# Kernel tuning notes

Measured on AMD Instinct MI355X. Metric: run time of the kernel, lower is better.

The kernel has to match this reference:

```python
import jax, jax.numpy as jnp
import numpy as np

B, T, D, H = 4, 1024, 1024, 16
DH = D // H  # 64

def setup_inputs() -> dict:
    key = jax.random.key(0)
    ks = jax.random.split(key, 5)
    s = 1.0 / np.sqrt(D)
    return {
        "x": jax.random.normal(ks[0], (B, T, D), dtype=jnp.float32),
        "Wqkv": jax.random.uniform(ks[1], (D, 3 * D), dtype=jnp.float32, minval=-s, maxval=s),
        "bqkv": jax.random.uniform(ks[2], (3 * D,), dtype=jnp.float32, minval=-s, maxval=s),
        "Wproj": jax.random.uniform(ks[3], (D, D), dtype=jnp.float32, minval=-s, maxval=s),
        "bproj": jax.random.uniform(ks[4], (D,), dtype=jnp.float32, minval=-s, maxval=s),
        "mask": jnp.ones((B, T), dtype=jnp.int32),
    }

def reference(x, Wqkv, bqkv, Wproj, bproj, mask):
    Bx, Tx, C = x.shape
    qkv = x @ Wqkv + bqkv                      # [B,T,3D]
    q, k, v = jnp.split(qkv, 3, axis=-1)
    # [B,H,T,DH]
    q = q.reshape(Bx, Tx, H, DH).transpose(0, 2, 1, 3)
    k = k.reshape(Bx, Tx, H, DH).transpose(0, 2, 1, 3)
    v = v.reshape(Bx, Tx, H, DH).transpose(0, 2, 1, 3)
    att = jnp.einsum("bhqd,bhkd->bhqk", q, k) / np.sqrt(DH)
    causal = jnp.tril(jnp.ones((Tx, Tx), dtype=bool))          # [T,T]
    keep = causal[None, None] & (mask[:, None, None, :] != 0)  # [B,1,T,T] broadcast
    att = jnp.where(keep, att, -jnp.inf)
    att = jax.nn.softmax(att, axis=-1)
    # dropout is identity in eval / p=0
    out = jnp.einsum("bhqk,bhkd->bhqd", att, v)                # [B,H,T,DH]
    out = out.transpose(0, 2, 1, 3).reshape(Bx, Tx, C)
    return out @ Wproj + bproj
```

## Files before the change

### kernel.cpp

```cpp
#include <hip/hip_runtime.h>
#include <hip/hip_bf16.h>
#include <cstddef>
#include <cstdint>

#define Bb 4
#define Tt 1024
#define Dd 1024
#define Hh 16

typedef __bf16 bf16x8 __attribute__((ext_vector_type(8)));
typedef __bf16 bf16x4 __attribute__((ext_vector_type(4)));
typedef float  f32x4  __attribute__((ext_vector_type(4)));

__device__ __forceinline__ void gload16(const void* g, void* l) {
    __builtin_amdgcn_global_load_lds(
        (const __attribute__((address_space(1))) void*)g,
        (__attribute__((address_space(3))) void*)l, 16, 0, 0);
}

__global__ __launch_bounds__(256) void prep(const float* __restrict__ x,
                                            const float* __restrict__ Wqkv,
                                            const float* __restrict__ Wproj,
                                            __bf16* __restrict__ xb,
                                            __bf16* __restrict__ wqT,
                                            __bf16* __restrict__ wpT) {
    const int bid = blockIdx.x;
    if (bid < 4096) {
        int i = bid * 256 + threadIdx.x;
        float4 v = ((const float4*)x)[i];
        bf16x4 o = { (__bf16)v.x, (__bf16)v.y, (__bf16)v.z, (__bf16)v.w };
        ((bf16x4*)xb)[i] = o;
        return;
    }
    __shared__ float ld[64][65];
    const float* in;
    __bf16* out;
    int K, N, k0, n0;
    if (bid < 4096 + 768) {
        int j = bid - 4096;
        in = Wqkv; out = wqT; K = 1024; N = 3072;
        k0 = (j & 15) * 64; n0 = (j >> 4) * 64;
    } else {
        int j = bid - 4096 - 768;
        in = Wproj; out = wpT; K = 1024; N = 1024;
        k0 = (j & 15) * 64; n0 = (j >> 4) * 64;
    }
    #pragma unroll
    for (int i = 0; i < 16; i++) {
        int idx = i * 256 + threadIdx.x;
        int r = idx >> 6, c = idx & 63;
        ld[r][c] = in[(size_t)(k0 + r) * N + n0 + c];
    }
    __syncthreads();
    #pragma unroll
    for (int i = 0; i < 16; i++) {
        int idx = i * 256 + threadIdx.x;
        int r = idx >> 6, c = idx & 63;
        out[(size_t)(n0 + r) * K + k0 + c] = (__bf16)ld[c][r];
    }
}

__device__ __forceinline__ void stage_half(const __bf16* __restrict__ g,
                                           __bf16* l, int tid) {
    #pragma unroll
    for (int s = 0; s < 2; ++s) {
        const int c = s * 512 + tid;
        const int r = c >> 3;
        const int seg = (c & 7) ^ (r & 7);
        gload16(&g[(size_t)r * 1024 + seg * 8], &l[c * 8]);
    }
}

template <int MH>
__device__ __forceinline__ void load_af(bf16x8 (&af)[4][2], const __bf16* AsC,
                                        int wy, int l15, int quad) {
    #pragma unroll
    for (int mi = 0; mi < 4; ++mi)
        #pragma unroll
        for (int kc = 0; kc < 2; ++kc)
            af[mi][kc] = *(const bf16x8*)&AsC[(wy * 128 + MH * 64 + mi * 16 + l15) * 64 +
                                              (((kc * 4 + quad) ^ (l15 & 7)) * 8)];
}

template <int MH, int NH>
__device__ __forceinline__ void mfma_quad(f32x4 (&acc)[8][4], const bf16x8 (&af)[4][2],
                                          const bf16x8 (&bf)[4][2]) {
    #pragma unroll
    for (int mi = 0; mi < 4; ++mi)
        #pragma unroll
        for (int nj = 0; nj < 2; ++nj) {
            f32x4 c = acc[MH * 4 + mi][NH * 2 + nj];
            c = __builtin_amdgcn_mfma_f32_16x16x32_bf16(af[mi][0], bf[NH * 2 + nj][0], c, 0, 0, 0);
            c = __builtin_amdgcn_mfma_f32_16x16x32_bf16(af[mi][1], bf[NH * 2 + nj][1], c, 0, 0, 0);
            acc[MH * 4 + mi][NH * 2 + nj] = c;
        }
}

__global__ __launch_bounds__(512, 2) void gemm_qkv(const __bf16* __restrict__ A,
                                                   const __bf16* __restrict__ Bt,
                                                   const float* __restrict__ bias,
                                                   __bf16* __restrict__ Cout,
                                                   __bf16* __restrict__ vt) {
    constexpr int N = 3072;
    constexpr int NT = 16;
    __shared__ __align__(16) __bf16 smem[65536];

    const int tid  = threadIdx.x;
    const int lane = tid & 63;
    const int wave = tid >> 6;
    const int wy = wave >> 2, wx = wave & 3;
    const int l15 = lane & 15, quad = lane >> 4;
    const size_t row0 = (size_t)blockIdx.y * 256;
    const size_t col0 = (size_t)blockIdx.x * 256;

    const __bf16* const Ab  = A  + row0 * 1024;
    const __bf16* const Bb_ = Bt + col0 * 1024;

    f32x4 acc[8][4] = {};
    bf16x8 af[4][2], bf[4][2];

    stage_half(Ab, smem, tid);
    stage_half(Ab + (size_t)128 * 1024, smem + 8192, tid);
    stage_half(Bb_, smem + 32768, tid);
    stage_half(Bb_ + (size_t)128 * 1024, smem + 32768 + 8192, tid);
    stage_half(Bb_ + 64, smem + 32768 + 16384, tid);
    stage_half(Bb_ + (size_t)128 * 1024 + 64, smem + 32768 + 16384 + 8192, tid);
    stage_half(Ab + 64, smem + 16384, tid);
    asm volatile("s_waitcnt vmcnt(6)" ::: "memory");
    __builtin_amdgcn_s_barrier();

    for (int t = 0; t < NT; ++t) {
        const int cur = t & 1;
        __bf16* const AsC = smem + cur * 16384;
        __bf16* const BsC = smem + 32768 + cur * 16384;
        __bf16* const AsN = smem + (cur ^ 1) * 16384;

        load_af<0>(af, AsC, wy, l15, quad);
        #pragma unroll
        for (int nj = 0; nj < 4; ++nj)
            #pragma unroll
            for (int kc = 0; kc < 2; ++kc)
                bf[nj][kc] = *(const bf16x8*)&BsC[(wx * 64 + nj * 16 + l15) * 64 +
                                                  (((kc * 4 + quad) ^ (l15 & 7)) * 8)];
        if (t + 1 < NT) stage_half(Ab + (size_t)128 * 1024 + (t + 1) * 64, AsN + 8192, tid);
        __builtin_amdgcn_s_barrier();
        asm volatile("s_waitcnt lgkmcnt(0)" ::: "memory");
        __builtin_amdgcn_s_setprio(1);
        mfma_quad<0, 0>(acc, af, bf);
        __builtin_amdgcn_s_setprio(0);
        __builtin_amdgcn_s_barrier();

        if (t + 2 < NT) stage_half(Bb_ + (t + 2) * 64, BsC, tid);
        __builtin_amdgcn_s_barrier();
        asm volatile("s_waitcnt lgkmcnt(0)" ::: "memory");
        __builtin_amdgcn_s_setprio(1);
        mfma_quad<0, 1>(acc, af, bf);
        __builtin_amdgcn_s_setprio(0);
        __builtin_amdgcn_s_barrier();

        load_af<1>(af, AsC, wy, l15, quad);
        if (t + 2 < NT) stage_half(Bb_ + (size_t)128 * 1024 + (t + 2) * 64, BsC + 8192, tid);
        __builtin_amdgcn_s_barrier();
        asm volatile("s_waitcnt lgkmcnt(0)" ::: "memory");
        __builtin_amdgcn_s_setprio(1);
        mfma_quad<1, 0>(acc, af, bf);
        __builtin_amdgcn_s_setprio(0);
        __builtin_amdgcn_s_barrier();

        if (t + 2 < NT) stage_half(Ab + (t + 2) * 64, AsC, tid);
        if (t + 2 < NT) {
            asm volatile("s_waitcnt vmcnt(6)" ::: "memory");
        } else if (t + 1 < NT) {
            asm volatile("s_waitcnt vmcnt(0)" ::: "memory");
        }
        __builtin_amdgcn_s_barrier();
        asm volatile("s_waitcnt lgkmcnt(0)" ::: "memory");
        __builtin_amdgcn_s_setprio(1);
        mfma_quad<1, 1>(acc, af, bf);
        __builtin_amdgcn_s_setprio(0);
        __builtin_amdgcn_s_barrier();
    }

    const float scale = (col0 < 1024) ? 0.125f : 1.0f;
    const int isV = (col0 >= 2048);
    for (int sl = 0; sl < 2; ++sl) {
        if (wy == sl) {
            #pragma unroll
            for (int nj = 0; nj < 4; ++nj) {
                const int cl = wx * 64 + nj * 16 + l15;
                const float bj = bias[col0 + cl];
                #pragma unroll
                for (int mi = 0; mi < 8; ++mi) {
                    #pragma unroll
                    for (int r = 0; r < 4; ++r)
                        smem[(mi * 16 + quad * 4 + r) * 264 + cl] =
                            (__bf16)((acc[mi][nj][r] + bj) * scale);
                }
            }
        }
        __syncthreads();
        #pragma unroll
        for (int p = 0; p < 8; ++p) {
            const int idx = p * 512 + tid;
            const int row = idx >> 5, ch = idx & 31;
            bf16x8 v = *(const bf16x8*)&smem[row * 264 + ch * 8];
            *(bf16x8*)&Cout[(row0 + sl * 128 + row) * N + col0 + ch * 8] = v;
        }
        if (isV) {
            const int bidx = (int)(row0 >> 10);
            const int t0g  = (int)(row0 & 1023) + sl * 128;
            const int cl   = tid & 255;
            const int th   = tid >> 8;
            const int hd   = (int)(col0 - 2048) + cl;
            const size_t vrow = ((size_t)((bidx * Hh + (hd >> 6)) * 64 + (hd & 63))) * Tt + t0g;
            #pragma unroll
            for (int p = 0; p < 8; ++p) {
                const int tch = th * 8 + p;
                bf16x8 v;
                #pragma unroll
                for (int u = 0; u < 8; ++u) v[u] = smem[(tch * 8 + u) * 264 + cl];
                *(bf16x8*)&vt[vrow + tch * 8] = v;
            }
        }
        __syncthreads();
    }
}

__global__ __launch_bounds__(256) void gemm_bf16_n64(const __bf16* __restrict__ A,
                                                     const __bf16* __restrict__ Bt,
                                                     const float* __restrict__ bias,
                                                     float* __restrict__ Cout,
                                                     int M, int N, int K) {
    __shared__ __align__(16) __bf16 As[128 * 64];
    __shared__ __align__(16) __bf16 Bs[64 * 64];
    const int tid  = threadIdx.x;
    const int lane = tid & 63;
    const int wave = tid >> 6;
    const int wy = wave >> 1, wx = wave & 1;
    const int l15 = lane & 15, quad = lane >> 4;
    const size_t row0 = (size_t)blockIdx.y * 128;
    const size_t col0 = (size_t)blockIdx.x * 64;

    f32x4 acc[4][2] = {};

    for (int k0 = 0; k0 < K; k0 += 64) {
        #pragma unroll
        for (int i = 0; i < 4; i++) {
            int c = i * 256 + tid;
            int r = c >> 3, seg = (c & 7) ^ (r & 7);
            gload16(&A[(row0 + r) * K + k0 + seg * 8], &As[c * 8]);
        }
        #pragma unroll
        for (int i = 0; i < 2; i++) {
            int c = i * 256 + tid;
            int r = c >> 3, seg = (c & 7) ^ (r & 7);
            gload16(&Bt[(col0 + r) * K + k0 + seg * 8], &Bs[c * 8]);
        }
        __syncthreads();
        #pragma unroll
        for (int kc = 0; kc < 2; kc++) {
            bf16x8 af[4], bfr[2];
            #pragma unroll
            for (int i = 0; i < 4; i++)
                af[i] = *(const bf16x8*)&As[(wy * 64 + i * 16 + l15) * 64 +
                                            (((kc * 4 + quad) ^ (l15 & 7)) * 8)];
            #pragma unroll
            for (int j = 0; j < 2; j++)
                bfr[j] = *(const bf16x8*)&Bs[(wx * 32 + j * 16 + l15) * 64 +
                                             (((kc * 4 + quad) ^ (l15 & 7)) * 8)];
            #pragma unroll
            for (int i = 0; i < 4; i++)
                #pragma unroll
                for (int j = 0; j < 2; j++)
                    acc[i][j] = __builtin_amdgcn_mfma_f32_16x16x32_bf16(af[i], bfr[j], acc[i][j], 0, 0, 0);
        }
        __syncthreads();
    }

    #pragma unroll
    for (int j = 0; j < 2; j++) {
        const size_t col = col0 + wx * 32 + j * 16 + l15;
        const float bj = bias[col];
        #pragma unroll
        for (int i = 0; i < 4; i++) {
            const size_t row = row0 + wy * 64 + i * 16 + quad * 4;
            #pragma unroll
            for (int r = 0; r < 4; r++)
                Cout[(row + r) * N + col] = acc[i][j][r] + bj;
        }
    }
}

__global__ __launch_bounds__(256, 4) void attn_mfma(const __bf16* __restrict__ qkv,
                                                    const __bf16* __restrict__ vt,
                                                    const int* __restrict__ mask,
                                                    __bf16* __restrict__ att) {
    __shared__ __align__(16) __bf16 Ks[2][4096];
    __shared__ __align__(16) __bf16 Vs[2][4096];
    __shared__ __align__(16) __bf16 Ps[4][1024];

    const int h  = blockIdx.x & 15;
    const int b  = blockIdx.x >> 4;
    const int qt = 15 - blockIdx.y;
    const int tid = threadIdx.x, lane = tid & 63, wave = tid >> 6;
    const int l15 = lane & 15, quad = lane >> 4;

    #pragma unroll
    for (int i = 0; i < 2; i++) {
        int c = i * 256 + tid;
        int rr = c >> 3, ch = c & 7;
        gload16(&qkv[((size_t)(b * Tt + qt * 64 + rr)) * 3072 + h * 64 + ((ch ^ (rr & 7)) * 8)],
                &Ks[0][c * 8]);
    }

    uint32_t mlo = 0, mhi = 0;
    for (int p = 0; p < 16; p++) {
        unsigned long long bal = __ballot(mask[b * Tt + p * 64 + lane] != 0);
        if ((lane & 15) == p) { mlo = (uint32_t)bal; mhi = (uint32_t)(bal >> 32); }
    }

    __syncthreads();
    bf16x8 qf0 = *(const bf16x8*)&Ks[0][(wave * 16 + l15) * 64 + ((quad ^ (l15 & 7)) * 8)];
    bf16x8 qf1 = *(const bf16x8*)&Ks[0][(wave * 16 + l15) * 64 + (((4 + quad) ^ (l15 & 7)) * 8)];
    __syncthreads();

    #pragma unroll
    for (int i = 0; i < 2; i++) {
        int c = i * 256 + tid;
        int rr = c >> 3, ch = c & 7, sw = ((ch ^ (rr & 7)) * 8);
        gload16(&qkv[((size_t)(b * Tt + rr)) * 3072 + 1024 + h * 64 + sw], &Ks[0][c * 8]);
        gload16(&vt[((size_t)((b * Hh + h) * 64 + rr)) * Tt + sw], &Vs[0][c * 8]);
    }

    f32x4 Oacc[4] = {};
    float lsum = 0.0f;

    for (int kt = 0; kt <= qt; kt++) {
        __syncthreads();
        const int cur = kt & 1;
        if (kt < qt) {
            #pragma unroll
            for (int i = 0; i < 2; i++) {
                int c = i * 256 + tid;
                int rr = c >> 3, ch = c & 7, sw = ((ch ^ (rr & 7)) * 8);
                gload16(&qkv[((size_t)(b * Tt + (kt + 1) * 64 + rr)) * 3072 + 1024 + h * 64 + sw],
                        &Ks[cur ^ 1][c * 8]);
                gload16(&vt[((size_t)((b * Hh + h) * 64 + rr)) * Tt + (kt + 1) * 64 + sw],
                        &Vs[cur ^ 1][c * 8]);
            }
        }

        const uint32_t lo = (uint32_t)__builtin_amdgcn_readlane((int)mlo, kt);
        const uint32_t hi = (uint32_t)__builtin_amdgcn_readlane((int)mhi, kt);

        bf16x8 ak[4][2];
        #pragma unroll
        for (int j = 0; j < 4; j++)
            #pragma unroll
            for (int kc = 0; kc < 2; kc++)
                ak[j][kc] = *(const bf16x8*)&Ks[cur][(j * 16 + l15) * 64 +
                                                     (((kc * 4 + quad) ^ (l15 & 7)) * 8)];
        #pragma unroll
        for (int j = 0; j < 4; j++) {
            f32x4 st = {};
            st = __builtin_amdgcn_mfma_f32_16x16x32_bf16(ak[j][0], qf0, st, 0, 0, 0);
            st = __builtin_amdgcn_mfma_f32_16x16x32_bf16(ak[j][1], qf1, st, 0, 0, 0);
            const uint32_t fld = (j < 2) ? (lo >> (j * 16)) : (hi >> ((j - 2) * 16));
            bf16x4 pv;
            #pragma unroll
            for (int r = 0; r < 4; r++) {
                const int tloc = j * 16 + quad * 4 + r;
                bool keep = (fld >> (quad * 4 + r)) & 1;
                if (kt == qt) keep = keep && (tloc <= wave * 16 + l15);
                const float pe = keep ? __expf(st[r]) : 0.0f;
                lsum += pe;
                pv[r] = (__bf16)pe;
            }
            *(bf16x4*)&Ps[wave][l15 * 64 + (((j * 4 + quad) ^ ((l15 & 7) << 1)) * 4)] = pv;
        }

        bf16x8 av[4][2];
        #pragma unroll
        for (int n = 0; n < 4; n++)
            #pragma unroll
            for (int kc = 0; kc < 2; kc++)
                av[n][kc] = *(const bf16x8*)&Vs[cur][(n * 16 + l15) * 64 +
                                                     (((kc * 4 + quad) ^ (l15 & 7)) * 8)];
        bf16x8 p0 = *(const bf16x8*)&Ps[wave][l15 * 64 + (((2 * quad) ^ ((l15 & 7) << 1)) * 4)];
        bf16x8 p1 = *(const bf16x8*)&Ps[wave][l15 * 64 + (((2 * (4 + quad)) ^ ((l15 & 7) << 1)) * 4)];
        #pragma unroll
        for (int n = 0; n < 4; n++) {
            Oacc[n] = __builtin_amdgcn_mfma_f32_16x16x32_bf16(av[n][0], p0, Oacc[n], 0, 0, 0);
            Oacc[n] = __builtin_amdgcn_mfma_f32_16x16x32_bf16(av[n][1], p1, Oacc[n], 0, 0, 0);
        }
    }

    float lt = lsum;
    lt += __shfl_xor(lt, 16);
    lt += __shfl_xor(lt, 32);
    const float inv = 1.0f / lt;
    const int q = qt * 64 + wave * 16 + l15;
    #pragma unroll
    for (int n = 0; n < 4; n++) {
        bf16x4 o;
        #pragma unroll
        for (int r = 0; r < 4; r++) o[r] = (__bf16)(Oacc[n][r] * inv);
        *(bf16x4*)&att[((size_t)(b * Tt + q)) * Dd + h * 64 + n * 16 + quad * 4] = o;
    }
}

extern "C" void kernel_launch(void* const* d_in, const int* in_sizes, int n_in,
                              void* d_out, int out_size, void* d_ws, size_t ws_size,
                              hipStream_t stream) {
    const float* x     = (const float*)d_in[0];
    const float* Wqkv  = (const float*)d_in[1];
    const float* bqkv  = (const float*)d_in[2];
    const float* Wproj = (const float*)d_in[3];
    const float* bproj = (const float*)d_in[4];
    const int*   mask  = (const int*)d_in[5];
    float* out = (float*)d_out;

    __bf16* xb  = (__bf16*)d_ws;
    __bf16* wqT = xb  + (size_t)4096 * 1024;
    __bf16* wpT = wqT + (size_t)3072 * 1024;
    __bf16* qkv = wpT + (size_t)1024 * 1024;
    __bf16* vt  = qkv + (size_t)4096 * 3072;
    __bf16* att = vt  + (size_t)4 * 16 * 64 * 1024;

    prep<<<4096 + 768 + 256, 256, 0, stream>>>(x, Wqkv, Wproj, xb, wqT, wpT);

    gemm_qkv<<<dim3(12, 16), 512, 0, stream>>>(xb, wqT, bqkv, qkv, vt);

    attn_mfma<<<dim3(64, 16), 256, 0, stream>>>(qkv, vt, mask, att);

    gemm_bf16_n64<<<dim3(16, 32), 256, 0, stream>>>(att, wpT, bproj, out, 4096, 1024, 1024);
}
```

Before: 166.8 us.

## Software-pipeline LDS fragment loads in QKV GEMM with partial lgkmcnt waits

Restructures the QKV GEMM main loop so the A fragments for the next K-step are prefetched from LDS during the last MFMA quadrant, B fragments are split into two halves, and partial lgkmcnt waits replace full drains. Staging addresses are precomputed once and sched_barriers pin instruction order. Barriers per iteration drop, and the two B halves are now staged together. The aim is to overlap LDS reads with MFMA and cut synchronization stalls, at the cost of more registers and tighter correctness constraints on wait counts.

```diff
diff --git a/kernel.cpp b/kernel.cpp
--- a/kernel.cpp
+++ b/kernel.cpp
@@ -17,6 +17,14 @@
         (const __attribute__((address_space(1))) void*)g,
         (__attribute__((address_space(3))) void*)l, 16, 0, 0);
 }
+
+#define LGKM4() asm volatile("s_waitcnt lgkmcnt(4)" ::: "memory")
+#define LGKM8() asm volatile("s_waitcnt lgkmcnt(8)" ::: "memory")
+#define LGKM0() asm volatile("s_waitcnt lgkmcnt(0)" ::: "memory")
+#define VMC6()  asm volatile("s_waitcnt vmcnt(6)" ::: "memory")
+#define VMC0()  asm volatile("s_waitcnt vmcnt(0)" ::: "memory")
+#define SB()    __builtin_amdgcn_s_barrier()
+#define SCB()   __builtin_amdgcn_sched_barrier(0)
 
 __global__ __launch_bounds__(256) void prep(const float* __restrict__ x,
                                             const float* __restrict__ Wqkv,
@@ -60,39 +68,31 @@
     }
 }
 
-__device__ __forceinline__ void stage_half(const __bf16* __restrict__ g,
-                                           __bf16* l, int tid) {
-    #pragma unroll
-    for (int s = 0; s < 2; ++s) {
-        const int c = s * 512 + tid;
-        const int r = c >> 3;
-        const int seg = (c & 7) ^ (r & 7);
-        gload16(&g[(size_t)r * 1024 + seg * 8], &l[c * 8]);
-    }
-}
-
-template <int MH>
-__device__ __forceinline__ void load_af(bf16x8 (&af)[4][2], const __bf16* AsC,
-                                        int wy, int l15, int quad) {
+__device__ __forceinline__ void ld8(bf16x8 (&f)[4][2], const __bf16* p0, const __bf16* p1) {
+    #pragma unroll
+    for (int mi = 0; mi < 4; ++mi) {
+        f[mi][0] = *(const bf16x8*)(p0 + mi * 1024);
+        f[mi][1] = *(const bf16x8*)(p1 + mi * 1024);
+    }
+}
+__device__ __forceinline__ void ld4(bf16x8 (&f)[2][2], const __bf16* p0, const __bf16* p1) {
+    #pragma unroll
+    for (int j = 0; j < 2; ++j) {
+        f[j][0] = *(const bf16x8*)(p0 + j * 1024);
+        f[j][1] = *(const bf16x8*)(p1 + j * 1024);
+    }
+}
+template <int M0, int N0>
+__device__ __forceinline__ void mm8(f32x4 (&acc)[8][4], const bf16x8 (&AF)[4][2],
+                                    const bf16x8 (&BF)[2][2]) {
     #pragma unroll
     for (int mi = 0; mi < 4; ++mi)
         #pragma unroll
-        for (int kc = 0; kc < 2; ++kc)
-            af[mi][kc] = *(const bf16x8*)&AsC[(wy * 128 + MH * 64 + mi * 16 + l15) * 64 +
-                                              (((kc * 4 + quad) ^ (l15 & 7)) * 8)];
-}
-
-template <int MH, int NH>
-__device__ __forceinline__ void mfma_quad(f32x4 (&acc)[8][4], const bf16x8 (&af)[4][2],
-                                          const bf16x8 (&bf)[4][2]) {
-    #pragma unroll
-    for (int mi = 0; mi < 4; ++mi)
-        #pragma unroll
-        for (int nj = 0; nj < 2; ++nj) {
-            f32x4 c = acc[MH * 4 + mi][NH * 2 + nj];
-            c = __builtin_amdgcn_mfma_f32_16x16x32_bf16(af[mi][0], bf[NH * 2 + nj][0], c, 0, 0, 0);
-            c = __builtin_amdgcn_mfma_f32_16x16x32_bf16(af[mi][1], bf[NH * 2 + nj][1], c, 0, 0, 0);
-            acc[MH * 4 + mi][NH * 2 + nj] = c;
+        for (int j = 0; j < 2; ++j) {
+            f32x4 c = acc[M0 + mi][N0 + j];
+            c = __builtin_amdgcn_mfma_f32_16x16x32_bf16(AF[mi][0], BF[j][0], c, 0, 0, 0);
+            c = __builtin_amdgcn_mfma_f32_16x16x32_bf16(AF[mi][1], BF[j][1], c, 0, 0, 0);
+            acc[M0 + mi][N0 + j] = c;
         }
 }
 
@@ -116,18 +116,34 @@
     const __bf16* const Ab  = A  + row0 * 1024;
     const __bf16* const Bb_ = Bt + col0 * 1024;
 
+    const int c0 = tid, c1 = 512 + tid;
+    const int r0 = c0 >> 3, s0 = ((c0 & 7) ^ (r0 & 7));
+    const int r1 = c1 >> 3, s1 = ((c1 & 7) ^ (r1 & 7));
+    const int go0 = r0 * 1024 + s0 * 8, go1 = r1 * 1024 + s1 * 8;
+    const int lo0 = c0 * 8, lo1 = c1 * 8;
+#define STAGE(gb, lb) do { const __bf16* _g = (gb); __bf16* _l = (lb); \
+        gload16(_g + go0, _l + lo0); gload16(_g + go1, _l + lo1); } while (0)
+
+    const int x7 = l15 & 7;
+    const int ch0 = (quad ^ x7) * 8, ch1 = ((4 + quad) ^ x7) * 8;
+    const int aoff0 = (wy * 128 + l15) * 64 + ch0;
+    const int aoff1 = (wy * 128 + l15) * 64 + ch1;
+    const int boff0 = (wx * 64 + l15) * 64 + ch0;
+    const int boff1 = (wx * 64 + l15) * 64 + ch1;
+
     f32x4 acc[8][4] = {};
-    bf16x8 af[4][2], bf[4][2];
-
-    stage_half(Ab, smem, tid);
-    stage_half(Ab + (size_t)128 * 1024, smem + 8192, tid);
-    stage_half(Bb_, smem + 32768, tid);
-    stage_half(Bb_ + (size_t)128 * 1024, smem + 32768 + 8192, tid);
-    stage_half(Bb_ + 64, smem + 32768 + 16384, tid);
-    stage_half(Bb_ + (size_t)128 * 1024 + 64, smem + 32768 + 16384 + 8192, tid);
-    stage_half(Ab + 64, smem + 16384, tid);
-    asm volatile("s_waitcnt vmcnt(6)" ::: "memory");
-    __builtin_amdgcn_s_barrier();
+    bf16x8 af0[4][2], af1[4][2], bfA[2][2], bfB[2][2];
+
+    STAGE(Ab,                          smem);
+    STAGE(Ab  + (size_t)128 * 1024,    smem + 8192);
+    STAGE(Bb_,                         smem + 32768);
+    STAGE(Bb_ + (size_t)128 * 1024,    smem + 32768 + 8192);
+    STAGE(Bb_ + 64,                    smem + 32768 + 16384);
+    STAGE(Bb_ + (size_t)128 * 1024 + 64, smem + 32768 + 16384 + 8192);
+    STAGE(Ab  + 64,                    smem + 16384);
+    VMC6(); SB(); SCB();
+    ld8(af0, smem + aoff0, smem + aoff1);
+    SCB();
 
     for (int t = 0; t < NT; ++t) {
         const int cur = t & 1;
@@ -135,51 +151,48 @@
         __bf16* const BsC = smem + 32768 + cur * 16384;
         __bf16* const AsN = smem + (cur ^ 1) * 16384;
 
-        load_af<0>(af, AsC, wy, l15, quad);
-        #pragma unroll
-        for (int nj = 0; nj < 4; ++nj)
-            #pragma unroll
-            for (int kc = 0; kc < 2; ++kc)
-                bf[nj][kc] = *(const bf16x8*)&BsC[(wx * 64 + nj * 16 + l15) * 64 +
-                                                  (((kc * 4 + quad) ^ (l15 & 7)) * 8)];
-        if (t + 1 < NT) stage_half(Ab + (size_t)128 * 1024 + (t + 1) * 64, AsN + 8192, tid);
-        __builtin_amdgcn_s_barrier();
-        asm volatile("s_waitcnt lgkmcnt(0)" ::: "memory");
+        ld4(bfA, BsC + boff0, BsC + boff1);
+        SCB();
+        ld4(bfB, BsC + 2048 + boff0, BsC + 2048 + boff1);
+        if (t + 1 < NT) STAGE(Ab + (size_t)128 * 1024 + (t + 1) * 64, AsN + 8192);
+        LGKM4(); SCB();
         __builtin_amdgcn_s_setprio(1);
-        mfma_quad<0, 0>(acc, af, bf);
+        mm8<0, 0>(acc, af0, bfA);
         __builtin_amdgcn_s_setprio(0);
-        __builtin_amdgcn_s_barrier();
-
-        if (t + 2 < NT) stage_half(Bb_ + (t + 2) * 64, BsC, tid);
-        __builtin_amdgcn_s_barrier();
-        asm volatile("s_waitcnt lgkmcnt(0)" ::: "memory");
+        SB(); SCB();
+
+        ld8(af1, AsC + 4096 + aoff0, AsC + 4096 + aoff1);
+        LGKM8(); SCB();
         __builtin_amdgcn_s_setprio(1);
-        mfma_quad<0, 1>(acc, af, bf);
+        mm8<0, 2>(acc, af0, bfB);
         __builtin_amdgcn_s_setprio(0);
-        __builtin_amdgcn_s_barrier();
-
-        load_af<1>(af, AsC, wy, l15, quad);
-        if (t + 2 < NT) stage_half(Bb_ + (size_t)128 * 1024 + (t + 2) * 64, BsC + 8192, tid);
-        __builtin_amdgcn_s_barrier();
-        asm volatile("s_waitcnt lgkmcnt(0)" ::: "memory");
+        SB(); SCB();
+
+        if (t + 2 < NT) {
+            STAGE(Bb_ + (t + 2) * 64, BsC);
+            STAGE(Bb_ + (size_t)128 * 1024 + (t + 2) * 64, BsC + 8192);
+        }
+        LGKM0(); SCB();
         __builtin_amdgcn_s_setprio(1);
-        mfma_quad<1, 0>(acc, af, bf);
+        mm8<4, 0>(acc, af1, bfA);
         __builtin_amdgcn_s_setprio(0);
-        __builtin_amdgcn_s_barrier();
-
-        if (t + 2 < NT) stage_half(Ab + (t + 2) * 64, AsC, tid);
+        SB(); SCB();
+
         if (t + 2 < NT) {
-            asm volatile("s_waitcnt vmcnt(6)" ::: "memory");
+            STAGE(Ab + (t + 2) * 64, AsC);
+            VMC6();
         } else if (t + 1 < NT) {
-            asm volatile("s_waitcnt vmcnt(0)" ::: "memory");
-        }
-        __builtin_amdgcn_s_barrier();
-        asm volatile("s_waitcnt lgkmcnt(0)" ::: "memory");
+            VMC0();
+        }
+        SB(); SCB();
+        if (t + 1 < NT) ld8(af0, AsN + aoff0, AsN + aoff1);
+        SCB();
         __builtin_amdgcn_s_setprio(1);
-        mfma_quad<1, 1>(acc, af, bf);
+        mm8<4, 2>(acc, af1, bfB);
         __builtin_amdgcn_s_setprio(0);
-        __builtin_amdgcn_s_barrier();
-    }
+        SB(); SCB();
+    }
+#undef STAGE
 
     const float scale = (col0 < 1024) ? 0.125f : 1.0f;
     const int isV = (col0 >= 2048);
```

After: 165.3 us. About the same (-0.9%).
